# Optimization experiments

Measured on AMD Instinct MI355X. Metric: run time of the kernel, lower is better.

## Reference

```python
import jax, jax.numpy as jnp
from jax import lax
import numpy as np

V, E, NF = 50000, 300, 1          # vocab, embed_size, n_features
H = 256                            # hidden size (both layers)
B, TH, TB = 128, 32, 512           # batch, headline len, body len
NC = 4                             # n_classes


def setup_inputs() -> dict:
    key = jax.random.key(0)
    ks = jax.random.split(key, 24)
    emb = jax.random.normal(ks[0], (V, E), jnp.float32) * 0.1
    emb = emb.at[0].set(0.0)  # pad token -> zero row so seqlen masking is meaningful

    def make_ids(kid, klen, T):
        raw = jax.random.randint(kid, (B, T, NF), 1, V)
        lens = jax.random.randint(klen, (B,), max(T // 4, 1), T + 1)
        mask = jnp.arange(T)[None, :, None] < lens[:, None, None]
        return jnp.where(mask, raw, 0)

    headline_ids = make_ids(ks[1], ks[2], TH)
    body_ids = make_ids(ks[3], ks[4], TB)

    def gru_params(k, din, h):
        k1, k2 = jax.random.split(k, 2)
        s = 1.0 / np.sqrt(din + h)
        return (jax.random.normal(k1, (din + h, 2 * h), jnp.float32) * s,
                jnp.ones((2 * h,), jnp.float32),          # TF GRUCell gate bias init = 1.0
                jax.random.normal(k2, (din + h, h), jnp.float32) * s,
                jnp.zeros((h,), jnp.float32))

    D0 = NF * E
    hd0 = gru_params(ks[5], D0, H)
    hd1 = gru_params(ks[6], H, H)
    bd0 = gru_params(ks[7], D0, H)
    bd1 = gru_params(ks[8], H, H)

    W_pred = jax.random.normal(ks[9], (2 * H, NC), jnp.float32) * (1.0 / np.sqrt(2 * H))
    b_pred = jnp.zeros((NC,), jnp.float32)

    out = {"headline_ids": headline_ids, "body_ids": body_ids, "embeddings": emb,
           "W_pred": W_pred, "b_pred": b_pred}
    for pref, p in (("hd0", hd0), ("hd1", hd1), ("bd0", bd0), ("bd1", bd1)):
        out[pref + "_Wg"], out[pref + "_bg"], out[pref + "_Wc"], out[pref + "_bc"] = p
    return out


def _seq_length(x):
    # used = sign(max(|x|, axis=2)); seqlen = sum over time
    return jnp.sum(jnp.sign(jnp.max(jnp.abs(x), axis=2)), axis=1).astype(jnp.int32)


def _gru_layer(x, seqlen, Wg, bg, Wc, bc):
    # x: [B, T, D] -> outputs [B, T, H], final state [B, H]; dynamic_rnn semantics:
    # past seqlen, output is zero and state is copied through.
    Bsz, T, _ = x.shape
    Hh = Wc.shape[1]
    xt = jnp.swapaxes(x, 0, 1)  # [T, B, D]
    tids = jnp.arange(T)

    def step(h, inp):
        xi, t = inp
        xh = jnp.concatenate([xi, h], axis=-1)
        r, u = jnp.split(jax.nn.sigmoid(xh @ Wg + bg), 2, axis=-1)
        c = jnp.tanh(jnp.concatenate([xi, r * h], axis=-1) @ Wc + bc)
        nh = u * h + (1.0 - u) * c
        valid = (t < seqlen)[:, None]
        out = jnp.where(valid, nh, 0.0)
        h_next = jnp.where(valid, nh, h)
        return h_next, out

    h0 = jnp.zeros((Bsz, Hh), x.dtype)
    hf, outs = lax.scan(step, h0, (xt, tids))
    return jnp.swapaxes(outs, 0, 1), hf


def _stream(ids, emb, layers):
    x = emb[ids].reshape(ids.shape[0], ids.shape[1], -1)  # [B, T, NF*E]
    h = None
    for (Wg, bg, Wc, bc) in layers:
        sl = _seq_length(x)  # recomputed from current layer inputs, as in the source
        x, h = _gru_layer(x, sl, Wg, bg, Wc, bc)
    return h


def reference(headline_ids, body_ids, embeddings,
              hd0_Wg, hd0_bg, hd0_Wc, hd0_bc, hd1_Wg, hd1_bg, hd1_Wc, hd1_bc,
              bd0_Wg, bd0_bg, bd0_Wc, bd0_bc, bd1_Wg, bd1_bg, bd1_Wc, bd1_bc,
              W_pred, b_pred):
    h_head = _stream(headline_ids, embeddings,
                     [(hd0_Wg, hd0_bg, hd0_Wc, hd0_bc), (hd1_Wg, hd1_bg, hd1_Wc, hd1_bc)])
    h_body = _stream(body_ids, embeddings,
                     [(bd0_Wg, bd0_bg, bd0_Wc, bd0_bc), (bd1_Wg, bd1_bg, bd1_Wc, bd1_bc)])
    pred_input = jnp.concatenate([h_head, h_body], axis=1)  # [B, 2H]
    return pred_input @ W_pred + b_pred                      # [B, NC]
```

## Files before the change

### kernel.cpp

```cpp
#include <hip/hip_runtime.h>
#include <cstdint>
#include <cstddef>

#define H_    256
#define NG    768
#define BATCH 128
#define TH_   32
#define TB_   512
#define E_    300
#define RPB   16
#define NBLK  (BATCH / RPB)

typedef _Float16 half8 __attribute__((ext_vector_type(8)));
typedef float    floatx4 __attribute__((ext_vector_type(4)));

#define AS1 __attribute__((address_space(1)))
#define AS3 __attribute__((address_space(3)))

#define WC_LGKM0 0xC07F
#define WC_VM14  0x0F7E
#define WC_VM6   0x0F76
#define WC_VM0   0x0F70

__device__ __forceinline__ void d_bias(const float* bg, const float* bc,
                                       float* bias, int idx)
{
  bias[idx] = (idx < 2 * H_) ? bg[idx] : bc[idx - 2 * H_];
}

__device__ __forceinline__ void d_packw(const float* Wg, const float* Wc,
                                        int din, _Float16* wpk, int idx)
{
  int tile = idx >> 6, lane = idx & 63;
  int grp = tile >> 4, tt = tile & 15;
  int wv = tt >> 1, s = tt & 1;
  const float* W; int ncols, n0;
  if (grp == 0)      { W = Wg; ncols = 2 * H_; n0 = wv * 32 + s * 16; }
  else if (grp == 1) { W = Wg; ncols = 2 * H_; n0 = 256 + wv * 32 + s * 16; }
  else               { W = Wc; ncols = H_;     n0 = wv * 32 + s * 16; }
  int n = n0 + (lane & 15);
  int kb = (lane >> 4) * 8;
#pragma unroll
  for (int kt = 0; kt < 8; ++kt) {
    _Float16* dst = wpk + ((size_t)(tile * 8 + kt) * 64 + lane) * 8;
#pragma unroll
    for (int j = 0; j < 8; ++j)
      dst[j] = (_Float16)W[(size_t)(din + kt * 32 + kb + j) * ncols + n];
  }
}

__device__ __forceinline__ void d_packbx(const float* Wg, const float* Wc,
                                         int din, int KT, _Float16* out, int idx)
{
  int lane = idx & 63, tile = idx >> 6;
  int kt = tile / 48, nt = tile - kt * 48;
  int col = nt * 16 + (lane & 15);
  int k0 = kt * 32 + (lane >> 4) * 8;
  const float* W; int ncols, c2;
  if (col < 2 * H_) { W = Wg; ncols = 2 * H_; c2 = col; }
  else              { W = Wc; ncols = H_;     c2 = col - 2 * H_; }
  _Float16* dst = out + ((size_t)(kt * 48 + nt) * 64 + lane) * 8;
#pragma unroll
  for (int j = 0; j < 8; ++j) {
    int k = k0 + j;
    dst[j] = (k < din) ? (_Float16)W[(size_t)k * ncols + c2] : (_Float16)0.f;
  }
}

__global__ __launch_bounds__(256) void pack_all(
    const int* __restrict__ idsH, const int* __restrict__ idsB,
    int* __restrict__ seqH, int* __restrict__ seqB,
    const float* Wg0, const float* bg0, const float* Wc0, const float* bc0,
    const float* Wg1, const float* bg1, const float* Wc1, const float* bc1,
    const float* Wg2, const float* bg2, const float* Wc2, const float* bc2,
    const float* Wg3, const float* bg3, const float* Wc3, const float* bc3,
    float* bi0, float* bi1, float* bi2, float* bi3,
    _Float16* w0, _Float16* w1, _Float16* w2, _Float16* w3,
    _Float16* x0, _Float16* x1, _Float16* x2, _Float16* x3)
{
  int blk = blockIdx.x, tid = threadIdx.x;
  if (blk < 256) {
    __shared__ int red[256];
    const int* ids = (blk < 128) ? idsH : idsB;
    int T = (blk < 128) ? TH_ : TB_;
    int* seq = (blk < 128) ? seqH : seqB;
    int b = blk & 127;
    int cnt = 0;
    for (int t = tid; t < T; t += 256) cnt += (ids[b * T + t] != 0) ? 1 : 0;
    red[tid] = cnt;
    __syncthreads();
    for (int s = 128; s > 0; s >>= 1) {
      if (tid < s) red[tid] += red[tid + s];
      __syncthreads();
    }
    if (tid == 0) seq[b] = red[0];
    return;
  }
  int idx = (blk - 256) * 256 + tid;
  const float* Wg[4] = {Wg0, Wg1, Wg2, Wg3};
  const float* bg[4] = {bg0, bg1, bg2, bg3};
  const float* Wc[4] = {Wc0, Wc1, Wc2, Wc3};
  const float* bc[4] = {bc0, bc1, bc2, bc3};
  float* bi[4] = {bi0, bi1, bi2, bi3};
  _Float16* wp[4] = {w0, w1, w2, w3};
  _Float16* bx[4] = {x0, x1, x2, x3};
  const int din[4] = {E_, H_, E_, H_};
  const int KT[4] = {10, 8, 10, 8};
#pragma unroll
  for (int s = 0; s < 4; ++s) {
    if (idx < NG) { d_bias(bg[s], bc[s], bi[s], idx); return; }
    idx -= NG;
    if (idx < 48 * 64) { d_packw(Wg[s], Wc[s], din[s], wp[s], idx); return; }
    idx -= 48 * 64;
    int szx = KT[s] * 48 * 64;
    if (idx < szx) { d_packbx(Wg[s], Wc[s], din[s], KT[s], bx[s], idx); return; }
    idx -= szx;
  }
}

__global__ __launch_bounds__(256) void gemm_mfma(
    const float* __restrict__ Adir, const int* __restrict__ ids,
    const float* __restrict__ emb,
    const _Float16* __restrict__ Bpk, const float* __restrict__ bias,
    float* __restrict__ G, int K, int KT, int t0, int tcsh, int T)
{
  __shared__ __align__(16) _Float16 Al[2][64 * 40];
  __shared__ __align__(16) _Float16 Bl[2][8 * 512];
  const int tid = threadIdx.x;
  const int w = tid >> 6, lane = tid & 63;
  const int quad = lane >> 4, l15 = lane & 15;
  const int m0 = blockIdx.x * 64;
  const int n0 = blockIdx.y * 128;
  const int tc = 1 << tcsh;

  const int am = tid >> 2, akq = tid & 3;
  const int arow = m0 + am;
  const float* asrc;
  if (Adir) {
    asrc = Adir + (size_t)arow * K;
  } else {
    int b = arow >> tcsh, tl = arow & (tc - 1);
    asrc = emb + (size_t)ids[b * T + t0 + tl] * K;
  }

  float a8[8];
  auto loadA = [&](int kt) {
    int k0 = kt * 32 + akq * 8;
#pragma unroll
    for (int j = 0; j < 8; ++j) a8[j] = (k0 + j < K) ? asrc[k0 + j] : 0.f;
  };
  auto writeA = [&](int buf) {
    half8 v;
#pragma unroll
    for (int j = 0; j < 8; ++j) v[j] = (_Float16)a8[j];
    *(half8*)&Al[buf][am * 40 + akq * 8] = v;
  };
  auto stageB = [&](int kt, int buf) {
#pragma unroll
    for (int i = 0; i < 2; ++i) {
      int nt = (n0 >> 4) + w * 2 + i;
      const _Float16* src = Bpk + ((size_t)(kt * 48 + nt) * 64 + lane) * 8;
      __builtin_amdgcn_global_load_lds(
          (const AS1 unsigned int*)src,
          (AS3 unsigned int*)&Bl[buf][(w * 2 + i) * 512 + lane * 8], 16, 0, 0);
    }
  };

  loadA(0);
  stageB(0, 0);
  writeA(0);
  floatx4 acc[4][2] = {};

  for (int kt = 0; kt < KT; ++kt) {
    const int buf = kt & 1;
    __syncthreads();
    if (kt + 1 < KT) { loadA(kt + 1); stageB(kt + 1, buf ^ 1); }
    half8 bf0 = *(const half8*)&Bl[buf][(w * 2 + 0) * 512 + lane * 8];
    half8 bf1 = *(const half8*)&Bl[buf][(w * 2 + 1) * 512 + lane * 8];
#pragma unroll
    for (int st = 0; st < 4; ++st) {
      half8 af = *(const half8*)&Al[buf][(st * 16 + l15) * 40 + quad * 8];
      acc[st][0] = __builtin_amdgcn_mfma_f32_16x16x32_f16(af, bf0, acc[st][0], 0, 0, 0);
      acc[st][1] = __builtin_amdgcn_mfma_f32_16x16x32_f16(af, bf1, acc[st][1], 0, 0, 0);
    }
    if (kt + 1 < KT) writeA(buf ^ 1);
  }

  float bb[2] = { bias[n0 + w * 32 + l15], bias[n0 + w * 32 + 16 + l15] };
#pragma unroll
  for (int s = 0; s < 2; ++s) {
    int col = n0 + w * 32 + s * 16 + l15;
    int g = col >> 8, kk = col & 255;
    int ww = kk >> 5, ss = (kk >> 4) & 1, ll = kk & 15;
    int cc = 2 * g + ss;
#pragma unroll
    for (int st = 0; st < 4; ++st) {
#pragma unroll
      for (int r = 0; r < 4; ++r) {
        int grow = m0 + st * 16 + quad * 4 + r;
        int b = grow >> tcsh, tl = grow & (tc - 1);
        int rg = b >> 4, mm = b & 15, qb = mm >> 2, rb = mm & 3;
        G[((size_t)tl * BATCH + rg * RPB) * NG +
          ((ww * 6 + cc) * 64 + qb * 16 + ll) * 4 + rb] = acc[st][s][r] + bb[s];
      }
    }
  }
}

__global__ __launch_bounds__(512, 1) void gru_pers(
    const float* __restrict__ G0, const _Float16* __restrict__ W0,
    const int* __restrict__ q0, float* __restrict__ o0, float* __restrict__ s0,
    int t00, int tc0,
    const float* __restrict__ G1, const _Float16* __restrict__ W1,
    const int* __restrict__ q1, float* __restrict__ o1, float* __restrict__ s1,
    int t01, int tc1,
    const float* __restrict__ G2, const _Float16* __restrict__ W2,
    const int* __restrict__ q2, float* __restrict__ o2, float* __restrict__ s2,
    int t02, int tc2,
    const float* rA_A, const int* rA_ids, const _Float16* rA_B,
    const float* rA_bi, float* rA_G, int rA_K, int rA_KT, int rA_t0,
    int rA_nbx, int rA_nblk,
    const float* rB_A, const int* rB_ids, const _Float16* rB_B,
    const float* rB_bi, float* rB_G, int rB_K, int rB_KT, int rB_t0,
    int rB_nbx, int rB_nblk,
    const float* rC_A, const int* rC_ids, const _Float16* rC_B,
    const float* rC_bi, float* rC_G, int rC_K, int rC_KT, int rC_t0,
    int rC_nbx, int rC_nblk,
    const float* __restrict__ r_emb, int r_tcsh, int r_T)
{
  __shared__ __align__(16) char smem[114688];

  const int tid = threadIdx.x;

  if (blockIdx.x >= 3 * NBLK) {
    int rb = blockIdx.x - 3 * NBLK;
    const float* Adir; const int* ids; const _Float16* Bpk; const float* bias;
    float* G; int K, KT, t0, nbx;
    if (rb < rA_nblk) {
      Adir = rA_A; ids = rA_ids; Bpk = rA_B; bias = rA_bi; G = rA_G;
      K = rA_K; KT = rA_KT; t0 = rA_t0; nbx = rA_nbx;
    } else if (rb < rA_nblk + rB_nblk) {
      rb -= rA_nblk;
      Adir = rB_A; ids = rB_ids; Bpk = rB_B; bias = rB_bi; G = rB_G;
      K = rB_K; KT = rB_KT; t0 = rB_t0; nbx = rB_nbx;
    } else {
      rb -= rA_nblk + rB_nblk;
      Adir = rC_A; ids = rC_ids; Bpk = rC_B; bias = rC_bi; G = rC_G;
      K = rC_K; KT = rC_KT; t0 = rC_t0; nbx = rC_nbx;
    }
    const int half = tid >> 8;
    _Float16* Al = (_Float16*)(smem + half * 10240);
    _Float16* Bl = (_Float16*)(smem + 20480 + half * 16384);
    const int t256 = tid & 255;
    const int w4 = (tid >> 6) & 3, lane = tid & 63;
    const int quad = lane >> 4, l15 = lane & 15;
    const int tidx = rb * 2 + half;
    const int bx = tidx % nbx, by = tidx / nbx;
    const int m0 = bx * 64, n0 = by * 128;
    const int tc = 1 << r_tcsh;

    const int am = t256 >> 2, akq = t256 & 3;
    const int arow = m0 + am;
    const float* asrc;
    if (Adir) {
      asrc = Adir + (size_t)arow * K;
    } else {
      int ab = arow >> r_tcsh, atl = arow & (tc - 1);
      asrc = r_emb + (size_t)ids[ab * r_T + t0 + atl] * K;
    }

    float a8[8];
    auto loadA = [&](int kt) {
      int k0 = kt * 32 + akq * 8;
#pragma unroll
      for (int j = 0; j < 8; ++j) a8[j] = (k0 + j < K) ? asrc[k0 + j] : 0.f;
    };
    auto writeA = [&](int buf) {
      half8 v;
#pragma unroll
      for (int j = 0; j < 8; ++j) v[j] = (_Float16)a8[j];
      *(half8*)&Al[buf * 2560 + am * 40 + akq * 8] = v;
    };
    auto stageB = [&](int kt, int buf) {
#pragma unroll
      for (int i = 0; i < 2; ++i) {
        int nt = (n0 >> 4) + w4 * 2 + i;
        const _Float16* src = Bpk + ((size_t)(kt * 48 + nt) * 64 + lane) * 8;
        __builtin_amdgcn_global_load_lds(
            (const AS1 unsigned int*)src,
            (AS3 unsigned int*)&Bl[buf * 4096 + (w4 * 2 + i) * 512 + lane * 8],
            16, 0, 0);
      }
    };

    loadA(0);
    stageB(0, 0);
    writeA(0);
    floatx4 acc[4][2] = {};

    for (int kt = 0; kt < KT; ++kt) {
      const int buf = kt & 1;
      __syncthreads();
      if (kt + 1 < KT) { loadA(kt + 1); stageB(kt + 1, buf ^ 1); }
      half8 bf0 = *(const half8*)&Bl[buf * 4096 + (w4 * 2 + 0) * 512 + lane * 8];
      half8 bf1 = *(const half8*)&Bl[buf * 4096 + (w4 * 2 + 1) * 512 + lane * 8];
#pragma unroll
      for (int st = 0; st < 4; ++st) {
        half8 af = *(const half8*)&Al[buf * 2560 + (st * 16 + l15) * 40 + quad * 8];
        acc[st][0] = __builtin_amdgcn_mfma_f32_16x16x32_f16(af, bf0, acc[st][0], 0, 0, 0);
        acc[st][1] = __builtin_amdgcn_mfma_f32_16x16x32_f16(af, bf1, acc[st][1], 0, 0, 0);
      }
      if (kt + 1 < KT) writeA(buf ^ 1);
    }

    float bb[2] = { bias[n0 + w4 * 32 + l15], bias[n0 + w4 * 32 + 16 + l15] };
#pragma unroll
    for (int s = 0; s < 2; ++s) {
      int col = n0 + w4 * 32 + s * 16 + l15;
      int g = col >> 8, kk = col & 255;
      int ww = kk >> 5, ss = (kk >> 4) & 1, ll = kk & 15;
      int cc = 2 * g + ss;
#pragma unroll
      for (int st = 0; st < 4; ++st) {
#pragma unroll
        for (int r = 0; r < 4; ++r) {
          int grow = m0 + st * 16 + quad * 4 + r;
          int b = grow >> r_tcsh, tl = grow & (tc - 1);
          int rg2 = b >> 4, mm = b & 15, qb = mm >> 2, rb2 = mm & 3;
          G[((size_t)tl * BATCH + rg2 * RPB) * NG +
            ((ww * 6 + cc) * 64 + qb * 16 + ll) * 4 + rb2] = acc[st][s][r] + bb[s];
        }
      }
    }
    return;
  }

  _Float16* hpk = (_Float16*)smem;
  _Float16* rpk = (_Float16*)(smem + 8192);
  float* GsB = (float*)(smem + 16384);

  const int job = blockIdx.x >> 3, rg = blockIdx.x & 7;
  const float* G; const _Float16* Wsrc; const int* seq;
  float* outp; float* state; int t0, tcl;
  if (job == 0)      { G = G0; Wsrc = W0; seq = q0; outp = o0; state = s0; t0 = t00; tcl = tc0; }
  else if (job == 1) { G = G1; Wsrc = W1; seq = q1; outp = o1; state = s1; t0 = t01; tcl = tc1; }
  else               { G = G2; Wsrc = W2; seq = q2; outp = o2; state = s2; t0 = t02; tcl = tc2; }
  if (!G) return;

  const int w = tid >> 6, lane = tid & 63;
  const int quad = lane >> 4, l15 = lane & 15;

  floatx4 wg[4][8];
  floatx4 wc[2][8];
#pragma unroll
  for (int i = 0; i < 4; ++i) {
    const int tile = (i >> 1) * 16 + w * 2 + (i & 1);
#pragma unroll
    for (int kt = 0; kt < 8; ++kt) {
      wg[i][kt] = *(const floatx4*)&Wsrc[((size_t)(tile * 8 + kt) * 64 + lane) * 8];
      asm volatile("" : "+v"(wg[i][kt]));
    }
  }
#pragma unroll
  for (int i = 0; i < 2; ++i) {
    const int tile = 32 + w * 2 + i;
#pragma unroll
    for (int kt = 0; kt < 8; ++kt) {
      wc[i][kt] = *(const floatx4*)&Wsrc[((size_t)(tile * 8 + kt) * 64 + lane) * 8];
      asm volatile("" : "+a"(wc[i][kt]));
    }
  }

  int seq4[4];
#pragma unroll
  for (int r = 0; r < 4; ++r) seq4[r] = seq[rg * RPB + quad * 4 + r];
  int Smax = 0;
#pragma unroll
  for (int i = 0; i < 16; ++i) Smax = max(Smax, seq[rg * RPB + i]);
  int steps = Smax - t0;
  if (steps < 0) steps = 0;
  if (steps > tcl) steps = tcl;

  const int wbase = (w * 64 + quad * 2 + (l15 >> 3)) * 8 + (l15 & 7);
  const int rbase = (((quad >> 1) << 5) + ((l15 & 3) << 3) +
                     ((l15 >> 2) << 1) + (quad & 1)) * 8;

  float h_reg[2][4];
#pragma unroll
  for (int s = 0; s < 2; ++s)
#pragma unroll
    for (int r = 0; r < 4; ++r) {
      int row = quad * 4 + r, k = w * 32 + s * 16 + l15;
      float v = (t0 == 0) ? 0.f : state[(size_t)(rg * RPB + row) * H_ + k];
      h_reg[s][r] = v;
      hpk[wbase + s * 256 + r * 64] = (_Float16)v;
    }

  const float* gblk = G + (size_t)rg * RPB * NG + w * (6 * 256);
  float* ldsw = GsB + w * (6 * 256);
  auto stage = [&](int t, int buf) {
    const float* gp = gblk + (size_t)t * BATCH * NG;
    float* lp = ldsw + buf * 12288;
#pragma unroll
    for (int c = 0; c < 6; ++c) {
      __builtin_amdgcn_global_load_lds(
          (const AS1 unsigned int*)(gp + c * 256 + lane * 4),
          (AS3 unsigned int*)(lp + c * 256), 16, 0, 0);
    }
  };
  if (steps > 0) stage(0, 0);
  __syncthreads();

  const _Float16* hA = &hpk[rbase];
  const _Float16* rA = &rpk[rbase];

  for (int t = 0; t < steps; ++t) {
    const int buf = t & 1;
    const bool staged = (t + 1 < steps);
    if (staged) stage(t + 1, buf ^ 1);

    floatx4 acc[4] = {};
#pragma unroll
    for (int kt = 0; kt < 8; ++kt) {
      half8 a = *(const half8*)&hA[kt * 512];
#pragma unroll
      for (int s = 0; s < 4; ++s)
        acc[s] = __builtin_amdgcn_mfma_f32_16x16x32_f16(
            a, __builtin_bit_cast(half8, wg[s][kt]), acc[s], 0, 0, 0);
    }

    if (staged) {
      if (outp) __builtin_amdgcn_s_waitcnt(WC_VM14);
      else      __builtin_amdgcn_s_waitcnt(WC_VM6);
    } else {
      __builtin_amdgcn_s_waitcnt(WC_VM0);
    }

    floatx4 gA[4];
#pragma unroll
    for (int c = 0; c < 4; ++c)
      gA[c] = *(const floatx4*)&GsB[buf * 12288 + (w * 6 + c) * 256 + lane * 4];

#pragma unroll
    for (int s = 0; s < 2; ++s)
#pragma unroll
      for (int r = 0; r < 4; ++r) {
        float pre = acc[s][r] + gA[s][r];
        float g = __builtin_amdgcn_rcpf(1.f + __expf(-pre));
        rpk[wbase + s * 256 + r * 64] = (_Float16)(g * h_reg[s][r]);
      }
    float u_reg[2][4];
#pragma unroll
    for (int s = 0; s < 2; ++s)
#pragma unroll
      for (int r = 0; r < 4; ++r) {
        float pre = acc[2 + s][r] + gA[2 + s][r];
        u_reg[s][r] = __builtin_amdgcn_rcpf(1.f + __expf(-pre));
      }
    __builtin_amdgcn_s_waitcnt(WC_LGKM0);
    __builtin_amdgcn_s_barrier();

    floatx4 accB[2] = {};
#pragma unroll
    for (int kt = 0; kt < 8; ++kt) {
      half8 a = *(const half8*)&rA[kt * 512];
#pragma unroll
      for (int s = 0; s < 2; ++s)
        accB[s] = __builtin_amdgcn_mfma_f32_16x16x32_f16(
            a, __builtin_bit_cast(half8, wc[s][kt]), accB[s], 0, 0, 0);
    }
    floatx4 gB[2];
#pragma unroll
    for (int s = 0; s < 2; ++s)
      gB[s] = *(const floatx4*)&GsB[buf * 12288 + (w * 6 + 4 + s) * 256 + lane * 4];

#pragma unroll
    for (int s = 0; s < 2; ++s)
#pragma unroll
      for (int r = 0; r < 4; ++r) {
        int row = quad * 4 + r;
        float pre = accB[s][r] + gB[s][r];
        float c = 1.f - 2.f * __builtin_amdgcn_rcpf(1.f + __expf(2.f * pre));
        float u = u_reg[s][r];
        float hn = u * h_reg[s][r] + (1.f - u) * c;
        bool valid = (t0 + t) < seq4[r];
        hn = valid ? hn : h_reg[s][r];
        h_reg[s][r] = hn;
        hpk[wbase + s * 256 + r * 64] = (_Float16)hn;
        if (outp)
          outp[((size_t)(rg * RPB + row) * tcl + t) * H_ + (w * 32 + s * 16 + l15)] =
              valid ? hn : 0.f;
      }
    __builtin_amdgcn_s_waitcnt(WC_LGKM0);
    __builtin_amdgcn_s_barrier();
  }
#pragma unroll
  for (int s = 0; s < 2; ++s)
#pragma unroll
    for (int r = 0; r < 4; ++r)
      state[(size_t)(rg * RPB + quad * 4 + r) * H_ + (w * 32 + s * 16 + l15)] =
          h_reg[s][r];
}

__global__ __launch_bounds__(512) void pred_k(
    const float* __restrict__ hh, const float* __restrict__ hb,
    const float* __restrict__ Wp, const float* __restrict__ bpred,
    float* __restrict__ out)
{
  int tid = threadIdx.x;
  int b = tid >> 2, c = tid & 3;
  float acc = bpred[c];
  for (int k = 0; k < H_; ++k) acc += hh[b * H_ + k] * Wp[k * 4 + c];
  for (int k = 0; k < H_; ++k) acc += hb[b * H_ + k] * Wp[(H_ + k) * 4 + c];
  out[b * 4 + c] = acc;
}

extern "C" void kernel_launch(void* const* d_in, const int* in_sizes, int n_in,
                              void* d_out, int out_size, void* d_ws, size_t ws_size,
                              hipStream_t stream)
{
  (void)in_sizes; (void)n_in; (void)out_size;
  const int*   idsH = (const int*)  d_in[0];
  const int*   idsB = (const int*)  d_in[1];
  const float* emb  = (const float*)d_in[2];
  const float* Wp   = (const float*)d_in[3];
  const float* bp   = (const float*)d_in[4];
  const float* W[4][4];
  for (int s = 0; s < 4; ++s)
    for (int q = 0; q < 4; ++q)
      W[s][q] = (const float*)d_in[5 + s * 4 + q];

  auto rnd = [](size_t n) { return (n + 255) & ~(size_t)255; };
  const size_t prefix_f =
      2 * rnd(BATCH) + 4 * (rnd(NG) + rnd(98304) + rnd(122880)) +
      4 * rnd((size_t)BATCH * H_);
  auto need_full = [&]() -> size_t {
    size_t s = prefix_f;
    s += 2 * rnd((size_t)BATCH * 32 * NG);
    s += 2 * rnd((size_t)BATCH * 32 * NG);
    s += 2 * rnd((size_t)BATCH * 32 * H_);
    s += 2 * rnd((size_t)BATCH * TH_ * NG);
    s += rnd((size_t)BATCH * TH_ * H_);
    return s * 4;
  };
  auto need_r2 = [&](int ch, bool rider) -> size_t {
    size_t s = prefix_f;
    s += rnd((size_t)BATCH * ch * NG) * (rider ? 2 : 1);
    s += rnd((size_t)BATCH * ch * NG);
    s += rnd((size_t)BATCH * ch * H_);
    s += rnd((size_t)BATCH * TH_ * NG);
    s += rnd((size_t)BATCH * TH_ * H_);
    return s * 4;
  };

  enum { M_FULL, M_R2, M_SERIAL } mode;
  int CH = 64; bool rider = false;
  if (need_full() <= ws_size) { mode = M_FULL; CH = 32; }
  else if (need_r2(64, true) <= ws_size) { mode = M_R2; CH = 64; rider = true; }
  else {
    CH = 64;
    while (CH > 8 && need_r2(CH, false) > ws_size) CH >>= 1;
    mode = (CH >= TH_) ? M_R2 : M_SERIAL;
  }
  const int CHH = (CH < TH_) ? CH : TH_;
  const int tcshB = __builtin_ctz(CH), tcshH = __builtin_ctz(CHH);

  float* wbase = (float*)d_ws;
  size_t off = 0;
  auto alloc = [&](size_t n) {
    float* p = wbase + off; off += rnd(n); return p;
  };
  int* seqH = (int*)alloc(BATCH);
  int* seqB = (int*)alloc(BATCH);
  float* bi[4]; _Float16* Wpk[4]; _Float16* Bxh[4];
  const int KT[4]  = {10, 8, 10, 8};
  for (int s = 0; s < 4; ++s) {
    bi[s]  = alloc(NG);
    Wpk[s] = (_Float16*)alloc(98304);
    Bxh[s] = (_Float16*)alloc(122880);
  }
  float* st0  = alloc((size_t)BATCH * H_);
  float* stH0 = alloc((size_t)BATCH * H_);
  float* hfH  = alloc((size_t)BATCH * H_);
  float* hfB  = alloc((size_t)BATCH * H_);

  float *Gc0b[2], *Gc1b[2], *Ocb[2], *GH0, *GH1, *OcH;
  if (mode == M_FULL) {
    Gc0b[0] = alloc((size_t)BATCH * CH * NG);
    Gc0b[1] = alloc((size_t)BATCH * CH * NG);
    Gc1b[0] = alloc((size_t)BATCH * CH * NG);
    Gc1b[1] = alloc((size_t)BATCH * CH * NG);
    Ocb[0]  = alloc((size_t)BATCH * CH * H_);
    Ocb[1]  = alloc((size_t)BATCH * CH * H_);
    GH0     = alloc((size_t)BATCH * TH_ * NG);
    GH1     = alloc((size_t)BATCH * TH_ * NG);
    OcH     = alloc((size_t)BATCH * TH_ * H_);
  } else {
    Gc0b[0] = alloc((size_t)BATCH * CH * NG);
    Gc0b[1] = rider ? alloc((size_t)BATCH * CH * NG) : Gc0b[0];
    Gc1b[0] = Gc1b[1] = alloc((size_t)BATCH * CH * NG);
    Ocb[0]  = Ocb[1]  = alloc((size_t)BATCH * CH * H_);
    GH1     = alloc((size_t)BATCH * TH_ * NG);
    OcH     = alloc((size_t)BATCH * TH_ * H_);
    GH0     = Gc1b[0];
  }

  {
    int packN = 0;
    for (int s = 0; s < 4; ++s) packN += NG + 48 * 64 + KT[s] * 48 * 64;
    int grid = 256 + (packN + 255) / 256;
    pack_all<<<grid, 256, 0, stream>>>(
        idsH, idsB, seqH, seqB,
        W[0][0], W[0][1], W[0][2], W[0][3],
        W[1][0], W[1][1], W[1][2], W[1][3],
        W[2][0], W[2][1], W[2][2], W[2][3],
        W[3][0], W[3][1], W[3][2], W[3][3],
        bi[0], bi[1], bi[2], bi[3],
        Wpk[0], Wpk[1], Wpk[2], Wpk[3],
        Bxh[0], Bxh[1], Bxh[2], Bxh[3]);
  }

  struct RJ {
    const float* A; const int* ids; const _Float16* B; const float* bi;
    float* G; int K, KT, t0, nbx, nblk;
  };
  auto gru_launch = [&](const float* g0, const _Float16* w0, const int* x0,
                        float* y0, float* z0, int a0, int b0,
                        const float* g1, const _Float16* w1, const int* x1,
                        float* y1, float* z1, int a1, int b1,
                        const float* g2, const _Float16* w2, const int* x2,
                        float* y2, float* z2, int a2, int b2,
                        RJ rA, RJ rB, RJ rC, int tcsh) {
    int grid = 3 * NBLK + rA.nblk + rB.nblk + rC.nblk;
    gru_pers<<<grid, 512, 0, stream>>>(
        g0, w0, x0, y0, z0, a0, b0,
        g1, w1, x1, y1, z1, a1, b1,
        g2, w2, x2, y2, z2, a2, b2,
        rA.A, rA.ids, rA.B, rA.bi, rA.G, rA.K, rA.KT, rA.t0, rA.nbx, rA.nblk,
        rB.A, rB.ids, rB.B, rB.bi, rB.G, rB.K, rB.KT, rB.t0, rB.nbx, rB.nblk,
        rC.A, rC.ids, rC.B, rC.bi, rC.G, rC.K, rC.KT, rC.t0, rC.nbx, rC.nblk,
        emb, tcsh, TB_);
  };
  const RJ RNULL = {nullptr, nullptr, nullptr, nullptr, nullptr, 0, 0, 0, 1, 0};

  if (mode == M_FULL) {
    const int nch = TB_ / CH;
    const int nbx = BATCH * CH / 64;
    const int nrb = nbx * (NG / 128) / 2;
    gemm_mfma<<<dim3(nbx, NG / 128), 256, 0, stream>>>(
        nullptr, idsB, emb, Bxh[2], bi[2], Gc0b[0], E_, KT[2], 0, tcshB, TB_);
    gemm_mfma<<<dim3(BATCH * TH_ / 64, NG / 128), 256, 0, stream>>>(
        nullptr, idsH, emb, Bxh[0], bi[0], GH0, E_, KT[0], 0, tcshH, TH_);

    for (int c = 0; c <= nch + 1; ++c) {
      const float* g0 = (c < nch) ? Gc0b[c & 1] : nullptr;
      const float* g1 = (c >= 2) ? Gc1b[c & 1] : nullptr;
      const float* g2 = (c == 0) ? GH0 : (c == 2) ? GH1 : nullptr;
      RJ rA = RNULL, rB = RNULL, rC = RNULL;
      if (c + 1 < nch)
        rA = {nullptr, idsB, Bxh[2], bi[2], Gc0b[(c + 1) & 1],
              E_, KT[2], (c + 1) * CH, nbx, nrb};
      if (c >= 1 && c <= nch)
        rB = {Ocb[(c - 1) & 1], nullptr, Bxh[3], bi[3], Gc1b[(c - 1) & 1],
              H_, KT[3], 0, nbx, nrb};
      if (c == 1)
        rC = {OcH, nullptr, Bxh[1], bi[1], GH1, H_, KT[1], 0,
              BATCH * TH_ / 64, (BATCH * TH_ / 64) * (NG / 128) / 2};

      gru_launch(
          g0, Wpk[2], seqB, (c < nch) ? Ocb[c & 1] : nullptr, st0, c * CH, CH,
          g1, Wpk[3], seqB, nullptr, hfB, (c - 2) * CH, CH,
          g2, Wpk[(c == 0) ? 0 : 1], seqH,
          (c == 0) ? OcH : nullptr, (c == 0) ? stH0 : hfH, 0, TH_,
          rA, rB, rC, tcshB);
    }
  } else if (mode == M_R2) {
    const int nch = TB_ / CH;
    const int nbx = BATCH * CH / 64;
    const int nrb = rider ? nbx * (NG / 128) / 2 : 0;
    dim3 ggH(BATCH * TH_ / 64, NG / 128);
    dim3 gg(nbx, NG / 128);
    gemm_mfma<<<ggH, 256, 0, stream>>>(nullptr, idsH, emb, Bxh[0], bi[0],
                                       GH0, E_, KT[0], 0, tcshH, TH_);
    gemm_mfma<<<gg, 256, 0, stream>>>(nullptr, idsB, emb, Bxh[2], bi[2],
                                      Gc0b[0], E_, KT[2], 0, tcshB, TB_);
    for (int c = 0; c < nch; ++c) {
      int t0 = c * CH;
      if (!rider && c > 0)
        gemm_mfma<<<gg, 256, 0, stream>>>(nullptr, idsB, emb, Bxh[2], bi[2],
                                          Gc0b[0], E_, KT[2], t0, tcshB, TB_);
      const float* g2 = (c == 0) ? GH0 : (c == 1) ? GH1 : nullptr;
      RJ rA = RNULL;
      if (rider && c + 1 < nch)
        rA = {nullptr, idsB, Bxh[2], bi[2], Gc0b[(c + 1) & 1],
              E_, KT[2], (c + 1) * CH, nbx, nrb};
      gru_launch(
          Gc0b[rider ? (c & 1) : 0], Wpk[2], seqB, Ocb[0], st0, t0, CH,
          (c > 0) ? Gc1b[0] : nullptr, Wpk[3], seqB, nullptr, hfB,
          (c - 1) * CH, CH,
          g2, Wpk[(c == 0) ? 0 : 1], seqH,
          (c == 0) ? OcH : nullptr, (c == 0) ? stH0 : hfH, 0, TH_,
          rA, RNULL, RNULL, tcshB);
      if (c == 0)
        gemm_mfma<<<ggH, 256, 0, stream>>>(OcH, nullptr, nullptr, Bxh[1], bi[1],
                                           GH1, H_, KT[1], 0, tcshH, TH_);
      gemm_mfma<<<gg, 256, 0, stream>>>(Ocb[0], nullptr, nullptr, Bxh[3], bi[3],
                                        Gc1b[0], H_, KT[3], 0, tcshB, TB_);
    }
    gru_launch(nullptr, Wpk[2], seqB, nullptr, st0, 0, CH,
               Gc1b[0], Wpk[3], seqB, nullptr, hfB, (nch - 1) * CH, CH,
               nullptr, Wpk[1], seqH, nullptr, hfH, 0, TH_,
               RNULL, RNULL, RNULL, tcshB);
  } else {
    auto run_stream = [&](const int* ids, int T, int chs, int tcsh,
                          const int* seq, int l0, int l1, float* hf) {
      int nchunks = T / chs;
      dim3 gg2(BATCH * chs / 64, NG / 128);
      for (int c = 0; c < nchunks; ++c) {
        int t0 = c * chs;
        gemm_mfma<<<gg2, 256, 0, stream>>>(nullptr, ids, emb, Bxh[l0], bi[l0],
                                           Gc0b[0], E_, KT[l0], t0, tcsh, T);
        gru_launch(Gc0b[0], Wpk[l0], seq, Ocb[0], st0, t0, chs,
                   (c > 0) ? Gc1b[0] : nullptr, Wpk[l1], seq, nullptr, hf,
                   (c - 1) * chs, chs,
                   nullptr, Wpk[l1], seq, nullptr, hf, 0, chs,
                   RNULL, RNULL, RNULL, tcsh);
        gemm_mfma<<<gg2, 256, 0, stream>>>(Ocb[0], nullptr, nullptr, Bxh[l1],
                                           bi[l1], Gc1b[0], H_, KT[l1], 0, tcsh, T);
      }
      gru_launch(nullptr, Wpk[l0], seq, nullptr, st0, 0, chs,
                 Gc1b[0], Wpk[l1], seq, nullptr, hf, (nchunks - 1) * chs, chs,
                 nullptr, Wpk[l1], seq, nullptr, hf, 0, chs,
                 RNULL, RNULL, RNULL, tcsh);
    };
    run_stream(idsH, TH_, CHH, tcshH, seqH, 0, 1, hfH);
    run_stream(idsB, TB_, CH,  tcshB, seqB, 2, 3, hfB);
  }

  pred_k<<<1, 512, 0, stream>>>(hfH, hfB, Wp, bp, (float*)d_out);
}
```

Baseline: 2.277 ms.

## Replace per-chunk kernel launches with a single cooperative persistent kernel

The full mode used to issue a chain of launches, one per 32-step chunk, each running the GRU recurrences plus rider GEMMs. This change fuses the whole schedule into one cooperative kernel of 256 blocks. GRU blocks and rider GEMM blocks advance through rounds separated by grid.sync, and the code falls back to the old dispatch if the cooperative launch fails. The aim is to remove launch and inter-kernel gap overhead, at the cost of grid-wide barriers and a fixed 256-block grid that must fit co-resident.

```diff
diff --git a/kernel.cpp b/kernel.cpp
--- a/kernel.cpp
+++ b/kernel.cpp
@@ -1,6 +1,9 @@
 #include <hip/hip_runtime.h>
+#include <hip/hip_cooperative_groups.h>
 #include <cstdint>
 #include <cstddef>
+
+namespace cg = cooperative_groups;
 
 #define H_    256
 #define NG    768
@@ -207,6 +210,338 @@
   }
 }
 
+__device__ __forceinline__ void rider_unit(
+    char* smem, int tid,
+    const float* Adir, const int* ids, const float* emb,
+    const _Float16* Bpk, const float* bias, float* G,
+    int K, int KT, int t0, int unit, int T)
+{
+  const int half = tid >> 8;
+  _Float16* Al = (_Float16*)(smem + half * 10240);
+  _Float16* Bl = (_Float16*)(smem + 20480 + half * 16384);
+  const int t256 = tid & 255;
+  const int w4 = (tid >> 6) & 3, lane = tid & 63;
+  const int quad = lane >> 4, l15 = lane & 15;
+  const int tidx = unit * 2 + half;
+  const int bx = tidx & 63, by = tidx >> 6;
+  const int m0 = bx * 64, n0 = by * 128;
+
+  const int am = t256 >> 2, akq = t256 & 3;
+  const int arow = m0 + am;
+  const float* asrc;
+  if (Adir) {
+    asrc = Adir + (size_t)arow * K;
+  } else {
+    int ab = arow >> 5, atl = arow & 31;
+    asrc = emb + (size_t)ids[ab * T + t0 + atl] * K;
+  }
+
+  float a8[8];
+  auto loadA = [&](int kt) {
+    int k0 = kt * 32 + akq * 8;
+#pragma unroll
+    for (int j = 0; j < 8; ++j) a8[j] = (k0 + j < K) ? asrc[k0 + j] : 0.f;
+  };
+  auto writeA = [&](int buf) {
+    half8 v;
+#pragma unroll
+    for (int j = 0; j < 8; ++j) v[j] = (_Float16)a8[j];
+    *(half8*)&Al[buf * 2560 + am * 40 + akq * 8] = v;
+  };
+  auto stageB = [&](int kt, int buf) {
+#pragma unroll
+    for (int i = 0; i < 2; ++i) {
+      int nt = (n0 >> 4) + w4 * 2 + i;
+      const _Float16* src = Bpk + ((size_t)(kt * 48 + nt) * 64 + lane) * 8;
+      __builtin_amdgcn_global_load_lds(
+          (const AS1 unsigned int*)src,
+          (AS3 unsigned int*)&Bl[buf * 4096 + (w4 * 2 + i) * 512 + lane * 8],
+          16, 0, 0);
+    }
+  };
+
+  loadA(0);
+  stageB(0, 0);
+  writeA(0);
+  floatx4 acc[4][2] = {};
+
+  for (int kt = 0; kt < KT; ++kt) {
+    const int buf = kt & 1;
+    __syncthreads();
+    if (kt + 1 < KT) { loadA(kt + 1); stageB(kt + 1, buf ^ 1); }
+    half8 bf0 = *(const half8*)&Bl[buf * 4096 + (w4 * 2 + 0) * 512 + lane * 8];
+    half8 bf1 = *(const half8*)&Bl[buf * 4096 + (w4 * 2 + 1) * 512 + lane * 8];
+#pragma unroll
+    for (int st = 0; st < 4; ++st) {
+      half8 af = *(const half8*)&Al[buf * 2560 + (st * 16 + l15) * 40 + quad * 8];
+      acc[st][0] = __builtin_amdgcn_mfma_f32_16x16x32_f16(af, bf0, acc[st][0], 0, 0, 0);
+      acc[st][1] = __builtin_amdgcn_mfma_f32_16x16x32_f16(af, bf1, acc[st][1], 0, 0, 0);
+    }
+    if (kt + 1 < KT) writeA(buf ^ 1);
+  }
+
+  float bb[2] = { bias[n0 + w4 * 32 + l15], bias[n0 + w4 * 32 + 16 + l15] };
+#pragma unroll
+  for (int s = 0; s < 2; ++s) {
+    int col = n0 + w4 * 32 + s * 16 + l15;
+    int g = col >> 8, kk = col & 255;
+    int ww = kk >> 5, ss = (kk >> 4) & 1, ll = kk & 15;
+    int cc = 2 * g + ss;
+#pragma unroll
+    for (int st = 0; st < 4; ++st) {
+#pragma unroll
+      for (int r = 0; r < 4; ++r) {
+        int grow = m0 + st * 16 + quad * 4 + r;
+        int b = grow >> 5, tl = grow & 31;
+        int rg2 = b >> 4, mm = b & 15, qb = mm >> 2, rb2 = mm & 3;
+        G[((size_t)tl * BATCH + rg2 * RPB) * NG +
+          ((ww * 6 + cc) * 64 + qb * 16 + ll) * 4 + rb2] = acc[st][s][r] + bb[s];
+      }
+    }
+  }
+}
+
+struct PersArgs {
+  const int *idsH, *idsB;
+  const float* emb;
+  const int *seqH, *seqB;
+  const _Float16 *Wpk0, *Wpk1, *Wpk2, *Wpk3;
+  const _Float16 *Bxh0, *Bxh1, *Bxh2, *Bxh3;
+  const float *bi0, *bi1, *bi2, *bi3;
+  float *Gc0b0, *Gc0b1, *Gc1b0, *Gc1b1, *Ocb0, *Ocb1;
+  float *GH0, *GH1, *OcH;
+  float *hfB, *hfH;
+};
+
+__global__ __launch_bounds__(512, 1) void fnc_pers(PersArgs A)
+{
+  __shared__ __align__(16) char smem[114688];
+  cg::grid_group grid = cg::this_grid();
+  const int bid = blockIdx.x, tid = threadIdx.x;
+  const bool is_rider = (bid >= 3 * NBLK);
+
+  _Float16* hpk = (_Float16*)smem;
+  _Float16* rpk = (_Float16*)(smem + 8192);
+  float* GsB = (float*)(smem + 16384);
+
+  const int job = bid >> 3, rg = bid & 7;
+  const int w = tid >> 6, lane = tid & 63;
+  const int quad = lane >> 4, l15 = lane & 15;
+
+  floatx4 wg[4][8];
+  floatx4 wc[2][8];
+  int seq4[4] = {0, 0, 0, 0};
+  int Smax = 0;
+  float h_reg[2][4];
+  const int wbase = (w * 64 + quad * 2 + (l15 >> 3)) * 8 + (l15 & 7);
+  const int rbase = (((quad >> 1) << 5) + ((l15 & 3) << 3) +
+                     ((l15 >> 2) << 1) + (quad & 1)) * 8;
+  const _Float16* hA = &hpk[rbase];
+  const _Float16* rA = &rpk[rbase];
+
+  auto loadW = [&](const _Float16* Wsrc) {
+#pragma unroll
+    for (int i = 0; i < 4; ++i) {
+      const int tile = (i >> 1) * 16 + w * 2 + (i & 1);
+#pragma unroll
+      for (int kt = 0; kt < 8; ++kt) {
+        wg[i][kt] = *(const floatx4*)&Wsrc[((size_t)(tile * 8 + kt) * 64 + lane) * 8];
+        asm volatile("" : "+v"(wg[i][kt]));
+      }
+    }
+#pragma unroll
+    for (int i = 0; i < 2; ++i) {
+      const int tile = 32 + w * 2 + i;
+#pragma unroll
+      for (int kt = 0; kt < 8; ++kt) {
+        wc[i][kt] = *(const floatx4*)&Wsrc[((size_t)(tile * 8 + kt) * 64 + lane) * 8];
+        asm volatile("" : "+a"(wc[i][kt]));
+      }
+    }
+  };
+
+  if (!is_rider) {
+    loadW(job == 0 ? A.Wpk2 : job == 1 ? A.Wpk3 : A.Wpk0);
+    const int* seq = (job == 2) ? A.seqH : A.seqB;
+#pragma unroll
+    for (int r = 0; r < 4; ++r) seq4[r] = seq[rg * RPB + quad * 4 + r];
+#pragma unroll
+    for (int i = 0; i < 16; ++i) Smax = max(Smax, seq[rg * RPB + i]);
+  }
+
+  for (int r = -1; r < 18; ++r) {
+    if (is_rider) {
+      int uA = (r + 1 < 16) ? 192 : 0;
+      int uB = (r >= 1 && r <= 16) ? 192 : 0;
+      int uH = (r == -1 || r == 1) ? 192 : 0;
+      int U = uA + uB + uH;
+      for (int u = bid - 3 * NBLK; u < U; u += 256 - 3 * NBLK) {
+        __syncthreads();
+        if (u < uA) {
+          rider_unit(smem, tid, nullptr, A.idsB, A.emb, A.Bxh2, A.bi2,
+                     ((r + 1) & 1) ? A.Gc0b1 : A.Gc0b0,
+                     E_, 10, (r + 1) * 32, u, TB_);
+        } else if (u < uA + uB) {
+          rider_unit(smem, tid, ((r - 1) & 1) ? A.Ocb1 : A.Ocb0, nullptr, A.emb,
+                     A.Bxh3, A.bi3, ((r - 1) & 1) ? A.Gc1b1 : A.Gc1b0,
+                     H_, 8, 0, u - uA, TB_);
+        } else if (r == -1) {
+          rider_unit(smem, tid, nullptr, A.idsH, A.emb, A.Bxh0, A.bi0,
+                     A.GH0, E_, 10, 0, u - uA - uB, TH_);
+        } else {
+          rider_unit(smem, tid, A.OcH, nullptr, A.emb, A.Bxh1, A.bi1,
+                     A.GH1, H_, 8, 0, u - uA - uB, TH_);
+        }
+      }
+    } else {
+      const float* G = nullptr; float* outp = nullptr; float* state = nullptr;
+      int t0 = 0;
+      if (job == 0) {
+        if (r >= 0 && r < 16) {
+          G = (r & 1) ? A.Gc0b1 : A.Gc0b0;
+          outp = (r & 1) ? A.Ocb1 : A.Ocb0;
+          t0 = r * 32;
+        }
+      } else if (job == 1) {
+        if (r >= 2) {
+          G = (r & 1) ? A.Gc1b1 : A.Gc1b0;
+          state = A.hfB;
+          t0 = (r - 2) * 32;
+        }
+      } else {
+        if (r == 0)      { G = A.GH0; outp = A.OcH; t0 = 0; }
+        else if (r == 1) { loadW(A.Wpk1); }
+        else if (r == 2) { G = A.GH1; state = A.hfH; t0 = 0; }
+      }
+
+      if (G) {
+        int steps = Smax - t0;
+        if (steps < 0) steps = 0;
+        if (steps > 32) steps = 32;
+
+        if (t0 == 0) {
+#pragma unroll
+          for (int s = 0; s < 2; ++s)
+#pragma unroll
+            for (int rr = 0; rr < 4; ++rr) {
+              h_reg[s][rr] = 0.f;
+              hpk[wbase + s * 256 + rr * 64] = (_Float16)0.f;
+            }
+        }
+
+        const float* gblk = G + (size_t)rg * RPB * NG + w * (6 * 256);
+        float* ldsw = GsB + w * (6 * 256);
+        auto stage = [&](int t, int buf) {
+          const float* gp = gblk + (size_t)t * BATCH * NG;
+          float* lp = ldsw + buf * 12288;
+#pragma unroll
+          for (int c = 0; c < 6; ++c) {
+            __builtin_amdgcn_global_load_lds(
+                (const AS1 unsigned int*)(gp + c * 256 + lane * 4),
+                (AS3 unsigned int*)(lp + c * 256), 16, 0, 0);
+          }
+        };
+        if (steps > 0) stage(0, 0);
+        __syncthreads();
+
+        for (int t = 0; t < steps; ++t) {
+          const int buf = t & 1;
+          const bool staged = (t + 1 < steps);
+          if (staged) stage(t + 1, buf ^ 1);
+
+          floatx4 acc[4] = {};
+#pragma unroll
+          for (int kt = 0; kt < 8; ++kt) {
+            half8 a = *(const half8*)&hA[kt * 512];
+#pragma unroll
+            for (int s = 0; s < 4; ++s)
+              acc[s] = __builtin_amdgcn_mfma_f32_16x16x32_f16(
+                  a, __builtin_bit_cast(half8, wg[s][kt]), acc[s], 0, 0, 0);
+          }
+
+          if (staged) {
+            if (outp) __builtin_amdgcn_s_waitcnt(WC_VM14);
+            else      __builtin_amdgcn_s_waitcnt(WC_VM6);
+          } else {
+            __builtin_amdgcn_s_waitcnt(WC_VM0);
+          }
+
+          floatx4 gA[4];
+#pragma unroll
+          for (int c = 0; c < 4; ++c)
+            gA[c] = *(const floatx4*)&GsB[buf * 12288 + (w * 6 + c) * 256 + lane * 4];
+
+#pragma unroll
+          for (int s = 0; s < 2; ++s)
+#pragma unroll
+            for (int rr = 0; rr < 4; ++rr) {
+              float pre = acc[s][rr] + gA[s][rr];
+              float g = __builtin_amdgcn_rcpf(1.f + __expf(-pre));
+              rpk[wbase + s * 256 + rr * 64] = (_Float16)(g * h_reg[s][rr]);
+            }
+          float u_reg[2][4];
+#pragma unroll
+          for (int s = 0; s < 2; ++s)
+#pragma unroll
+            for (int rr = 0; rr < 4; ++rr) {
+              float pre = acc[2 + s][rr] + gA[2 + s][rr];
+              u_reg[s][rr] = __builtin_amdgcn_rcpf(1.f + __expf(-pre));
+            }
+          __builtin_amdgcn_s_waitcnt(WC_LGKM0);
+          __builtin_amdgcn_s_barrier();
+
+          floatx4 accB[2] = {};
+#pragma unroll
+          for (int kt = 0; kt < 8; ++kt) {
+            half8 a = *(const half8*)&rA[kt * 512];
+#pragma unroll
+            for (int s = 0; s < 2; ++s)
+              accB[s] = __builtin_amdgcn_mfma_f32_16x16x32_f16(
+                  a, __builtin_bit_cast(half8, wc[s][kt]), accB[s], 0, 0, 0);
+          }
+          floatx4 gB[2];
+#pragma unroll
+          for (int s = 0; s < 2; ++s)
+            gB[s] = *(const floatx4*)&GsB[buf * 12288 + (w * 6 + 4 + s) * 256 + lane * 4];
+
+#pragma unroll
+          for (int s = 0; s < 2; ++s)
+#pragma unroll
+            for (int rr = 0; rr < 4; ++rr) {
+              int row = quad * 4 + rr;
+              float pre = accB[s][rr] + gB[s][rr];
+              float c = 1.f - 2.f * __builtin_amdgcn_rcpf(1.f + __expf(2.f * pre));
+              float u = u_reg[s][rr];
+              float hn = u * h_reg[s][rr] + (1.f - u) * c;
+              bool valid = (t0 + t) < seq4[rr];
+              hn = valid ? hn : h_reg[s][rr];
+              h_reg[s][rr] = hn;
+              hpk[wbase + s * 256 + rr * 64] = (_Float16)hn;
+              if (outp)
+                outp[((size_t)(rg * RPB + row) * 32 + t) * H_ + (w * 32 + s * 16 + l15)] =
+                    valid ? hn : 0.f;
+            }
+          __builtin_amdgcn_s_waitcnt(WC_LGKM0);
+          __builtin_amdgcn_s_barrier();
+        }
+
+        if (state) {
+#pragma unroll
+          for (int s = 0; s < 2; ++s)
+#pragma unroll
+            for (int rr = 0; rr < 4; ++rr)
+              state[(size_t)(rg * RPB + quad * 4 + rr) * H_ + (w * 32 + s * 16 + l15)] =
+                  h_reg[s][rr];
+        }
+      }
+    }
+
+    __threadfence();
+    grid.sync();
+    __threadfence();
+  }
+}
+
 __global__ __launch_bounds__(512, 1) void gru_pers(
     const float* __restrict__ G0, const _Float16* __restrict__ W0,
     const int* __restrict__ q0, float* __restrict__ o0, float* __restrict__ s0,
@@ -643,7 +978,7 @@
   };
   const RJ RNULL = {nullptr, nullptr, nullptr, nullptr, nullptr, 0, 0, 0, 1, 0};
 
-  if (mode == M_FULL) {
+  auto run_full_dispatch = [&]() {
     const int nch = TB_ / CH;
     const int nbx = BATCH * CH / 64;
     const int nrb = nbx * (NG / 128) / 2;
@@ -651,7 +986,6 @@
         nullptr, idsB, emb, Bxh[2], bi[2], Gc0b[0], E_, KT[2], 0, tcshB, TB_);
     gemm_mfma<<<dim3(BATCH * TH_ / 64, NG / 128), 256, 0, stream>>>(
         nullptr, idsH, emb, Bxh[0], bi[0], GH0, E_, KT[0], 0, tcshH, TH_);
-
     for (int c = 0; c <= nch + 1; ++c) {
       const float* g0 = (c < nch) ? Gc0b[c & 1] : nullptr;
       const float* g1 = (c >= 2) ? Gc1b[c & 1] : nullptr;
@@ -666,13 +1000,33 @@
       if (c == 1)
         rC = {OcH, nullptr, Bxh[1], bi[1], GH1, H_, KT[1], 0,
               BATCH * TH_ / 64, (BATCH * TH_ / 64) * (NG / 128) / 2};
-
       gru_launch(
           g0, Wpk[2], seqB, (c < nch) ? Ocb[c & 1] : nullptr, st0, c * CH, CH,
           g1, Wpk[3], seqB, nullptr, hfB, (c - 2) * CH, CH,
           g2, Wpk[(c == 0) ? 0 : 1], seqH,
           (c == 0) ? OcH : nullptr, (c == 0) ? stH0 : hfH, 0, TH_,
           rA, rB, rC, tcshB);
+    }
+  };
+
+  if (mode == M_FULL) {
+    PersArgs pa;
+    pa.idsH = idsH; pa.idsB = idsB; pa.emb = emb;
+    pa.seqH = seqH; pa.seqB = seqB;
+    pa.Wpk0 = Wpk[0]; pa.Wpk1 = Wpk[1]; pa.Wpk2 = Wpk[2]; pa.Wpk3 = Wpk[3];
+    pa.Bxh0 = Bxh[0]; pa.Bxh1 = Bxh[1]; pa.Bxh2 = Bxh[2]; pa.Bxh3 = Bxh[3];
+    pa.bi0 = bi[0]; pa.bi1 = bi[1]; pa.bi2 = bi[2]; pa.bi3 = bi[3];
+    pa.Gc0b0 = Gc0b[0]; pa.Gc0b1 = Gc0b[1];
+    pa.Gc1b0 = Gc1b[0]; pa.Gc1b1 = Gc1b[1];
+    pa.Ocb0 = Ocb[0]; pa.Ocb1 = Ocb[1];
+    pa.GH0 = GH0; pa.GH1 = GH1; pa.OcH = OcH;
+    pa.hfB = hfB; pa.hfH = hfH;
+    void* kargs[] = { (void*)&pa };
+    hipError_t e = hipLaunchCooperativeKernel(
+        (const void*)fnc_pers, dim3(256), dim3(512), kargs, 0, stream);
+    if (e != hipSuccess) {
+      (void)hipGetLastError();
+      run_full_dispatch();
     }
   } else if (mode == M_R2) {
     const int nch = TB_ / CH;
```

Result: slower. 5.442 ms (+139.0%).
